# Kernel tuning notes

Hardware: AMD Instinct MI355X
Metric: run time of the kernel (lower is better)

## Reference

```python
import jax, jax.numpy as jnp
import numpy as np

B, H, S, DK = 2, 16, 2048, 64


def setup_inputs() -> dict:
    key = jax.random.key(0)
    k1, k2, k3, k4 = jax.random.split(key, 4)
    Q = jax.random.normal(k1, (B, H, S, DK), dtype=jnp.float32)
    K = jax.random.normal(k2, (B, H, S, DK), dtype=jnp.float32)
    V = jax.random.normal(k3, (B, H, S, DK), dtype=jnp.float32)
    attn_mask = jax.random.randint(k4, (B, 1, S, S), 0, 2).astype(jnp.bool_)
    return {"Q": Q, "K": K, "V": V, "attn_mask": attn_mask}


def reference(Q, K, V, attn_mask):
    d_k = Q.shape[-1]
    scale = 1.0 / jnp.sqrt(jnp.asarray(d_k, dtype=Q.dtype))
    # scores: [B,H,S,S]
    scores = jnp.einsum('bhqd,bhkd->bhqk', Q, K) * scale
    scores = jnp.where(attn_mask, jnp.asarray(-1e9, dtype=scores.dtype), scores)
    attn = jax.nn.softmax(scores, axis=-1)
    # dropout in eval mode (identity) for deterministic reference
    return jnp.einsum('bhqk,bhkd->bhqd', attn, V)
```

## Files before the change

### kernel.cpp

```cpp
#include <hip/hip_runtime.h>
#include <hip/hip_bf16.h>

#define Bdim 2
#define Hdim 16
#define Sdim 2048
#define Ddim 64
#define KVBLK 64
#define NT (Sdim / KVBLK)
#define WQ 32
#define NWAVE 4
#define QTILE (WQ * NWAVE)
#define QSCL (0.125f * 1.44269504088896f)
#define SCALE 0.125f
#define BUFE 8192
#define VOFF 4096

typedef __bf16 bf16x8 __attribute__((ext_vector_type(8)));
typedef float  f32x4  __attribute__((ext_vector_type(4)));
typedef float  f32x16 __attribute__((ext_vector_type(16)));
typedef unsigned u32x4 __attribute__((ext_vector_type(4)));

__device__ __forceinline__ void gll16(const __bf16* g, __bf16* l) {
  __builtin_amdgcn_global_load_lds(
      (const __attribute__((address_space(1))) void*)g,
      (__attribute__((address_space(3))) void*)l, 16, 0, 0);
}
__device__ __forceinline__ unsigned cvtpk_raw(float lo, float hi) {
  unsigned r;
  asm("v_cvt_pk_bf16_f32 %0, %1, %2" : "=v"(r) : "v"(lo), "v"(hi));
  return r;
}
template <bool SW>
__device__ __forceinline__ unsigned pko(float a, float b) {
  return SW ? cvtpk_raw(b, a) : cvtpk_raw(a, b);
}
__device__ __forceinline__ unsigned cvtpk(float a, float b, bool sw) {
  const float lo = sw ? b : a;
  const float hi = sw ? a : b;
  return cvtpk_raw(lo, hi);
}
template <bool SW>
__device__ __forceinline__ void packAll(const float (&sv0)[16],
                                        const float (&sv1)[16],
                                        unsigned (&pw)[16]) {
#pragma unroll
  for (int ks = 0; ks < 4; ++ks) {
    const int rb = 8 * (ks & 1);
    if (ks < 2) {
      pw[ks * 4 + 0] = pko<SW>(sv0[rb + 0], sv0[rb + 1]);
      pw[ks * 4 + 1] = pko<SW>(sv0[rb + 2], sv0[rb + 3]);
      pw[ks * 4 + 2] = pko<SW>(sv0[rb + 4], sv0[rb + 5]);
      pw[ks * 4 + 3] = pko<SW>(sv0[rb + 6], sv0[rb + 7]);
    } else {
      pw[ks * 4 + 0] = pko<SW>(sv1[rb + 0], sv1[rb + 1]);
      pw[ks * 4 + 1] = pko<SW>(sv1[rb + 2], sv1[rb + 3]);
      pw[ks * 4 + 2] = pko<SW>(sv1[rb + 4], sv1[rb + 5]);
      pw[ks * 4 + 3] = pko<SW>(sv1[rb + 6], sv1[rb + 7]);
    }
  }
}

__global__ __launch_bounds__(256) void prep_all(
    const void* __restrict__ mask, unsigned long long* __restrict__ packed,
    const float* __restrict__ K, const float* __restrict__ V,
    __bf16* __restrict__ Kb, __bf16* __restrict__ Vt) {
  __shared__ __bf16 tile[64][72];
  const int t = threadIdx.x;

  if (blockIdx.x < 512) {
    const int nwords = Bdim * Sdim * (Sdim / 64);
    const unsigned* m32 = (const unsigned*)mask;
    const unsigned char* m8 = (const unsigned char*)mask;
    int gid = blockIdx.x * 256 + t;
    int lane = gid & 63;
    int wid = gid >> 6;
    const int nwaves = 512 * 256 / 64;
    bool isBytes = __any(m32[lane] > 1u);
    for (int w = wid; w < nwords; w += nwaves) {
      int v = isBytes ? (int)m8[(size_t)w * 64 + lane]
                      : (int)m32[(size_t)w * 64 + lane];
      unsigned long long bal = __ballot(v != 0);
      if (lane == 0) packed[w] = bal;
    }
    return;
  }

  const int idx = blockIdx.x - 512;
  const int bh = idx >> 5, st = idx & 31;
  const int r = t >> 2, c0 = (t & 3) << 4;
  {
    const float* ks = K + ((size_t)bh * Sdim + st * 64 + r) * Ddim + c0;
    bf16x8 o0, o1;
#pragma unroll
    for (int j = 0; j < 8; ++j) o0[j] = (__bf16)ks[j];
#pragma unroll
    for (int j = 0; j < 8; ++j) o1[j] = (__bf16)ks[8 + j];
    __bf16* kd = Kb + ((size_t)bh * Sdim + st * 64 + r) * Ddim + c0;
    *(bf16x8*)kd = o0;
    *(bf16x8*)(kd + 8) = o1;
  }
  {
    const float* vs = V + ((size_t)bh * Sdim + st * 64 + r) * Ddim + c0;
#pragma unroll
    for (int j = 0; j < 16; ++j) tile[r][c0 + j] = (__bf16)vs[j];
  }
  __syncthreads();
  {
    const int d = t >> 2, s0 = (t & 3) << 4;
    __bf16 o[16];
#pragma unroll
    for (int j = 0; j < 16; ++j) o[j] = tile[s0 + j][d];
    __bf16* dst = Vt + ((size_t)bh * Ddim + d) * Sdim + st * 64 + s0;
    *(bf16x8*)dst = *(bf16x8*)&o[0];
    *(bf16x8*)(dst + 8) = *(bf16x8*)&o[8];
  }
}

__global__ __launch_bounds__(256, 2) void attn5(
    const float* __restrict__ Q, const __bf16* __restrict__ Kb,
    const __bf16* __restrict__ Vt,
    const unsigned long long* __restrict__ maskP, float* __restrict__ Out) {
  __shared__ alignas(16) __bf16 sm[4 * BUFE];

  const int tid = threadIdx.x;
  const int lane = tid & 63;
  const int w = tid >> 6;
  const int l31 = lane & 31;
  const int hi = lane >> 5;
  const int rsw = l31 & 7;

  const int bid = blockIdx.x;
  const int bh = bid & 31;
  const int qt = bid >> 5;
  const int b = bh >> 4;
  const int qrow = qt * QTILE + w * WQ + l31;

  const __bf16* Kbase = Kb + (size_t)bh * Sdim * Ddim;
  const __bf16* Vbase = Vt + (size_t)bh * (size_t)Ddim * Sdim;
  const unsigned long long* mp =
      maskP + ((size_t)b * Sdim + qrow) * (Sdim / 64);

  const bool sw = (cvtpk_raw(0.0f, 1.0f) & 0xFFFFu) != 0u;

  bf16x8 qf[4];
  {
    const float* qs = Q + ((size_t)bh * Sdim + qrow) * Ddim;
#pragma unroll
    for (int step = 0; step < 4; ++step) {
      const int d0 = step * 16 + hi * 8;
      float4 a = *(const float4*)(qs + d0);
      float4 c = *(const float4*)(qs + d0 + 4);
      u32x4 f;
      f[0] = cvtpk(a.x * QSCL, a.y * QSCL, sw);
      f[1] = cvtpk(a.z * QSCL, a.w * QSCL, sw);
      f[2] = cvtpk(c.x * QSCL, c.y * QSCL, sw);
      f[3] = cvtpk(c.z * QSCL, c.w * QSCL, sw);
      qf[step] = __builtin_bit_cast(bf16x8, f);
    }
  }

  const int srow = 16 * w + (lane >> 3);
  const int sblk = (lane & 7) ^ ((lane >> 3) & 7);
  const int dstw = w * 1024;

#define STAGE(OFFE, kp_, vp_)                                   \
  do {                                                          \
    gll16((kp_), &sm[(OFFE) + dstw]);                           \
    gll16((kp_) + 8 * Ddim, &sm[(OFFE) + dstw + 512]);          \
    gll16((vp_), &sm[(OFFE) + VOFF + dstw]);                    \
    gll16((vp_) + 8 * Sdim, &sm[(OFFE) + VOFF + dstw + 512]);   \
  } while (0)

  f32x16 otA = {0,0,0,0,0,0,0,0,0,0,0,0,0,0,0,0};
  f32x16 otB = {0,0,0,0,0,0,0,0,0,0,0,0,0,0,0,0};
  float lrow = 0.f;

  unsigned long long mwCur = mp[0];
  {
    const __bf16* kp0 = Kbase + (size_t)srow * Ddim + sblk * 8;
    const __bf16* vp0 = Vbase + (size_t)srow * Sdim + sblk * 8;
    STAGE(0, kp0, vp0);
  }
  const __bf16* kpS = Kbase + (size_t)(KVBLK + srow) * Ddim + sblk * 8;
  const __bf16* vpS = Vbase + (size_t)srow * Sdim + KVBLK + sblk * 8;

#define ITER(RD, ST, KTN, LAST)                                                \
  do {                                                                         \
    unsigned long long mwNext = 0;                                             \
    if (!(LAST)) {                                                             \
      mwNext = mp[(KTN)];                                                      \
      STAGE((ST) * BUFE, kpS, vpS);                                            \
      kpS += (size_t)KVBLK * Ddim;                                             \
      vpS += KVBLK;                                                            \
      asm volatile("s_waitcnt vmcnt(5)" ::: "memory");                         \
    } else {                                                                   \
      asm volatile("s_waitcnt vmcnt(0)" ::: "memory");                         \
    }                                                                          \
    __builtin_amdgcn_s_barrier();                                              \
    __builtin_amdgcn_sched_barrier(0);                                         \
    f32x16 st0 = {0,0,0,0,0,0,0,0,0,0,0,0,0,0,0,0};                            \
    f32x16 st1 = {0,0,0,0,0,0,0,0,0,0,0,0,0,0,0,0};                            \
    __builtin_amdgcn_s_setprio(1);                                             \
    _Pragma("unroll") for (int step = 0; step < 4; ++step) {                   \
      bf16x8 kf = *(const bf16x8*)&sm[(RD) * BUFE + l31 * 64 +                 \
                                      (((step * 2 + hi) ^ rsw) << 3)];         \
      st0 = __builtin_amdgcn_mfma_f32_32x32x16_bf16(kf, qf[step], st0, 0,0,0); \
    }                                                                          \
    _Pragma("unroll") for (int step = 0; step < 4; ++step) {                   \
      bf16x8 kf = *(const bf16x8*)&sm[(RD) * BUFE + (32 + l31) * 64 +          \
                                      (((step * 2 + hi) ^ rsw) << 3)];         \
      st1 = __builtin_amdgcn_mfma_f32_32x32x16_bf16(kf, qf[step], st1, 0,0,0); \
    }                                                                          \
    __builtin_amdgcn_s_setprio(0);                                             \
    float sv0[16], sv1[16];                                                    \
    const unsigned w0s = ((unsigned)mwCur) >> (hi * 4);                        \
    const unsigned w1s = ((unsigned)(mwCur >> 32)) >> (hi * 4);                \
    _Pragma("unroll") for (int r = 0; r < 16; ++r) {                           \
      const int cr = (r & 3) + 8 * (r >> 2);                                   \
      const float e0 = __builtin_amdgcn_exp2f(st0[r]);                         \
      const float e1 = __builtin_amdgcn_exp2f(st1[r]);                         \
      sv0[r] = ((w0s >> cr) & 1u) ? 0.f : e0;                                  \
      sv1[r] = ((w1s >> cr) & 1u) ? 0.f : e1;                                  \
    }                                                                          \
    float s8[8];                                                               \
    _Pragma("unroll") for (int j = 0; j < 8; ++j)                              \
      s8[j] = (sv0[j] + sv0[j + 8]) + (sv1[j] + sv1[j + 8]);                   \
    lrow += ((s8[0] + s8[4]) + (s8[1] + s8[5])) +                              \
            ((s8[2] + s8[6]) + (s8[3] + s8[7]));                               \
    unsigned pw[16];                                                           \
    if (!sw) packAll<false>(sv0, sv1, pw);                                     \
    else     packAll<true>(sv0, sv1, pw);                                      \
    bf16x8 pb[4];                                                              \
    _Pragma("unroll") for (int ks = 0; ks < 4; ++ks) {                         \
      const unsigned W0 = pw[ks * 4 + 0], W1 = pw[ks * 4 + 1];                 \
      const unsigned X0 = pw[ks * 4 + 2], X1 = pw[ks * 4 + 3];                 \
      const unsigned s1 = hi ? W0 : X0;                                        \
      const unsigned s2 = hi ? W1 : X1;                                        \
      const unsigned r1 = __shfl_xor(s1, 32, 64);                              \
      const unsigned r2 = __shfl_xor(s2, 32, 64);                              \
      u32x4 wv;                                                                \
      wv[0] = hi ? r1 : W0;                                                    \
      wv[1] = hi ? r2 : W1;                                                    \
      wv[2] = hi ? X0 : r1;                                                    \
      wv[3] = hi ? X1 : r2;                                                    \
      pb[ks] = __builtin_bit_cast(bf16x8, wv);                                 \
    }                                                                          \
    __builtin_amdgcn_s_setprio(1);                                             \
    _Pragma("unroll") for (int ks = 0; ks < 4; ++ks) {                         \
      bf16x8 vf = *(const bf16x8*)&sm[(RD) * BUFE + VOFF + l31 * 64 +          \
                                      (((ks * 2 + hi) ^ rsw) << 3)];           \
      otA = __builtin_amdgcn_mfma_f32_32x32x16_bf16(vf, pb[ks], otA, 0,0,0);   \
    }                                                                          \
    _Pragma("unroll") for (int ks = 0; ks < 4; ++ks) {                         \
      bf16x8 vf = *(const bf16x8*)&sm[(RD) * BUFE + VOFF + (32 + l31) * 64 +   \
                                      (((ks * 2 + hi) ^ rsw) << 3)];           \
      otB = __builtin_amdgcn_mfma_f32_32x32x16_bf16(vf, pb[ks], otB, 0,0,0);   \
    }                                                                          \
    __builtin_amdgcn_s_setprio(0);                                             \
    if (!(LAST)) mwCur = mwNext;                                               \
  } while (0)

#pragma unroll 1
  for (int g = 0; g < 7; ++g) {
    ITER(0, 1, 4 * g + 1, false);
    ITER(1, 2, 4 * g + 2, false);
    ITER(2, 3, 4 * g + 3, false);
    ITER(3, 0, 4 * g + 4, false);
  }
  ITER(0, 1, 29, false);
  ITER(1, 2, 30, false);
  ITER(2, 3, 31, false);
  ITER(3, 0, 0, true);
#undef ITER
#undef STAGE

  lrow += __shfl_xor(lrow, 32, 64);
  const float inv = 1.f / (lrow + 1e-30f);
  float* orow = Out + ((size_t)bh * Sdim + qrow) * Ddim;
#pragma unroll
  for (int g = 0; g < 4; ++g) {
    const int d0 = 8 * g + 4 * hi;
    float4 va = {otA[4 * g] * inv, otA[4 * g + 1] * inv,
                 otA[4 * g + 2] * inv, otA[4 * g + 3] * inv};
    float4 vb = {otB[4 * g] * inv, otB[4 * g + 1] * inv,
                 otB[4 * g + 2] * inv, otB[4 * g + 3] * inv};
    *(float4*)(orow + d0) = va;
    *(float4*)(orow + 32 + d0) = vb;
  }
}

__global__ __launch_bounds__(256) void attn_fallback(
    const float* __restrict__ Q, const float* __restrict__ K,
    const float* __restrict__ V, const void* __restrict__ maskRaw,
    float* __restrict__ Out) {
  __shared__ alignas(16) __bf16 Kl[KVBLK * Ddim];
  __shared__ alignas(16) __bf16 Vts[Ddim * KVBLK];
  __shared__ alignas(16) __bf16 Pl[4][16 * 64];

  const int tid = threadIdx.x;
  const int lane = tid & 63;
  const int w = tid >> 6;
  const int lhi = lane >> 4;
  const int llo = lane & 15;

  const int qt = blockIdx.x;
  const int bh = blockIdx.y;
  const int b = bh >> 4;
  const int qbase = qt * 64;

  const float* Qp = Q + (size_t)bh * Sdim * Ddim;
  const float* Kp = K + (size_t)bh * Sdim * Ddim;
  const float* Vp = V + (size_t)bh * Sdim * Ddim;

  bool maskBytes = __any(((const unsigned*)maskRaw)[lane] > 1u);

  bf16x8 qf0, qf1;
  {
    const int qr = qbase + w * 16 + llo;
    const float* src = Qp + (size_t)qr * Ddim + lhi * 8;
#pragma unroll
    for (int i = 0; i < 8; ++i) qf0[i] = (__bf16)(src[i] * SCALE);
#pragma unroll
    for (int i = 0; i < 8; ++i) qf1[i] = (__bf16)(src[32 + i] * SCALE);
  }

  f32x4 acc[4] = {{0.f,0.f,0.f,0.f},{0.f,0.f,0.f,0.f},
                  {0.f,0.f,0.f,0.f},{0.f,0.f,0.f,0.f}};
  float mrow[4], lrw[4];
#pragma unroll
  for (int r = 0; r < 4; ++r) { mrow[r] = -3.0e38f; lrw[r] = 0.f; }

  for (int kt = 0; kt < NT; ++kt) {
    __syncthreads();
    {
      int r = tid >> 2;
      int c0 = (tid & 3) << 4;
      const float* ks = Kp + (size_t)(kt * KVBLK + r) * Ddim + c0;
      const float* vs = Vp + (size_t)(kt * KVBLK + r) * Ddim + c0;
      float kv[16], vv[16];
#pragma unroll
      for (int j = 0; j < 4; ++j) {
        *(float4*)(&kv[j * 4]) = *(const float4*)(ks + j * 4);
        *(float4*)(&vv[j * 4]) = *(const float4*)(vs + j * 4);
      }
      const int swzK = (r & 7) << 3;
      bf16x8 k0v, k1v;
#pragma unroll
      for (int j = 0; j < 8; ++j) { k0v[j] = (__bf16)kv[j]; k1v[j] = (__bf16)kv[8 + j]; }
      *(bf16x8*)&Kl[r * 64 + (c0 ^ swzK)] = k0v;
      *(bf16x8*)&Kl[r * 64 + ((c0 + 8) ^ swzK)] = k1v;
#pragma unroll
      for (int j = 0; j < 16; ++j) {
        int d = c0 + j;
        Vts[d * 64 + (r ^ ((d & 7) << 3))] = (__bf16)vv[j];
      }
    }
    __syncthreads();

    float sv[4][4];
#pragma unroll
    for (int cb = 0; cb < 4; ++cb) {
      int krow = cb * 16 + llo;
      int swz = (krow & 7) << 3;
      bf16x8 kf0 = *(const bf16x8*)&Kl[krow * 64 + ((lhi * 8) ^ swz)];
      bf16x8 kf1 = *(const bf16x8*)&Kl[krow * 64 + ((32 + lhi * 8) ^ swz)];
      f32x4 s = {0.f, 0.f, 0.f, 0.f};
      s = __builtin_amdgcn_mfma_f32_16x16x32_bf16(qf0, kf0, s, 0, 0, 0);
      s = __builtin_amdgcn_mfma_f32_16x16x32_bf16(qf1, kf1, s, 0, 0, 0);
#pragma unroll
      for (int r = 0; r < 4; ++r) {
        size_t q = qbase + w * 16 + lhi * 4 + r;
        size_t k = (size_t)kt * KVBLK + cb * 16 + llo;
        size_t idx = ((size_t)b * Sdim + q) * Sdim + k;
        bool masked = maskBytes ? (((const unsigned char*)maskRaw)[idx] != 0)
                                : (((const int*)maskRaw)[idx] != 0);
        sv[cb][r] = masked ? -1e9f : s[r];
      }
    }

    float corr[4], tsum[4];
#pragma unroll
    for (int r = 0; r < 4; ++r) {
      float mx = fmaxf(fmaxf(sv[0][r], sv[1][r]), fmaxf(sv[2][r], sv[3][r]));
#pragma unroll
      for (int off = 1; off < 16; off <<= 1)
        mx = fmaxf(mx, __shfl_xor(mx, off, 64));
      float mnew = fmaxf(mrow[r], mx);
      corr[r] = __expf(mrow[r] - mnew);
      mrow[r] = mnew;
      tsum[r] = 0.f;
    }
#pragma unroll
    for (int cb = 0; cb < 4; ++cb) {
#pragma unroll
      for (int r = 0; r < 4; ++r) {
        float p = __expf(sv[cb][r] - mrow[r]);
        tsum[r] += p;
        int row = lhi * 4 + r;
        int col = cb * 16 + llo;
        Pl[w][row * 64 + (col ^ ((row & 7) << 3))] = (__bf16)p;
      }
    }
#pragma unroll
    for (int r = 0; r < 4; ++r) {
      float s = tsum[r];
#pragma unroll
      for (int off = 1; off < 16; off <<= 1)
        s += __shfl_xor(s, off, 64);
      lrw[r] = lrw[r] * corr[r] + s;
#pragma unroll
      for (int db = 0; db < 4; ++db) acc[db][r] *= corr[r];
    }
    asm volatile("s_waitcnt lgkmcnt(0)" ::: "memory");

    bf16x8 pf0 = *(const bf16x8*)&Pl[w][llo * 64 + ((lhi * 8) ^ ((llo & 7) << 3))];
    bf16x8 pf1 = *(const bf16x8*)&Pl[w][llo * 64 + ((32 + lhi * 8) ^ ((llo & 7) << 3))];
#pragma unroll
    for (int db = 0; db < 4; ++db) {
      int d = db * 16 + llo;
      int swz = (d & 7) << 3;
      bf16x8 vf0 = *(const bf16x8*)&Vts[d * 64 + ((lhi * 8) ^ swz)];
      bf16x8 vf1 = *(const bf16x8*)&Vts[d * 64 + ((32 + lhi * 8) ^ swz)];
      acc[db] = __builtin_amdgcn_mfma_f32_16x16x32_bf16(pf0, vf0, acc[db], 0, 0, 0);
      acc[db] = __builtin_amdgcn_mfma_f32_16x16x32_bf16(pf1, vf1, acc[db], 0, 0, 0);
    }
  }

#pragma unroll
  for (int r = 0; r < 4; ++r) {
    float inv = 1.f / lrw[r];
    int q = qbase + w * 16 + lhi * 4 + r;
    float* dst = Out + ((size_t)bh * Sdim + q) * Ddim + llo;
#pragma unroll
    for (int db = 0; db < 4; ++db) dst[db * 16] = acc[db][r] * inv;
  }
}

extern "C" void kernel_launch(void* const* d_in, const int* in_sizes, int n_in,
                              void* d_out, int out_size, void* d_ws, size_t ws_size,
                              hipStream_t stream) {
  const float* Q = (const float*)d_in[0];
  const float* K = (const float*)d_in[1];
  const float* V = (const float*)d_in[2];
  const void* mask = d_in[3];
  float* out = (float*)d_out;

  const size_t packed_bytes =
      (size_t)Bdim * Sdim * (Sdim / 64) * sizeof(unsigned long long);
  const size_t tensor_bf16 = (size_t)Bdim * Hdim * Sdim * Ddim * 2;

  if (ws_size >= packed_bytes + 2 * tensor_bf16) {
    unsigned long long* packed = (unsigned long long*)d_ws;
    __bf16* Kb = (__bf16*)((char*)d_ws + packed_bytes);
    __bf16* Vt = (__bf16*)((char*)d_ws + packed_bytes + tensor_bf16);
    prep_all<<<512 + Bdim * Hdim * (Sdim / 64), 256, 0, stream>>>(
        mask, packed, K, V, Kb, Vt);
    attn5<<<(Sdim / QTILE) * Bdim * Hdim, 256, 0, stream>>>(Q, Kb, Vt, packed, out);
  } else {
    attn_fallback<<<dim3(Sdim / 64, Bdim * Hdim), 256, 0, stream>>>(Q, K, V, mask, out);
  }
}
```

Before: 96.32 us.

## Give each wave private double-buffered K/V LDS staging and drop block barriers

```diff
diff --git a/kernel.cpp b/kernel.cpp
--- a/kernel.cpp
+++ b/kernel.cpp
@@ -5,15 +5,13 @@
 #define Hdim 16
 #define Sdim 2048
 #define Ddim 64
-#define KVBLK 64
-#define NT (Sdim / KVBLK)
+#define NT2 64
 #define WQ 32
 #define NWAVE 4
 #define QTILE (WQ * NWAVE)
 #define QSCL (0.125f * 1.44269504088896f)
 #define SCALE 0.125f
-#define BUFE 8192
-#define VOFF 4096
+#define WREG 8192
 
 typedef __bf16 bf16x8 __attribute__((ext_vector_type(8)));
 typedef float  f32x4  __attribute__((ext_vector_type(4)));
@@ -40,23 +38,15 @@
   return cvtpk_raw(lo, hi);
 }
 template <bool SW>
-__device__ __forceinline__ void packAll(const float (&sv0)[16],
-                                        const float (&sv1)[16],
-                                        unsigned (&pw)[16]) {
-#pragma unroll
-  for (int ks = 0; ks < 4; ++ks) {
-    const int rb = 8 * (ks & 1);
-    if (ks < 2) {
-      pw[ks * 4 + 0] = pko<SW>(sv0[rb + 0], sv0[rb + 1]);
-      pw[ks * 4 + 1] = pko<SW>(sv0[rb + 2], sv0[rb + 3]);
-      pw[ks * 4 + 2] = pko<SW>(sv0[rb + 4], sv0[rb + 5]);
-      pw[ks * 4 + 3] = pko<SW>(sv0[rb + 6], sv0[rb + 7]);
-    } else {
-      pw[ks * 4 + 0] = pko<SW>(sv1[rb + 0], sv1[rb + 1]);
-      pw[ks * 4 + 1] = pko<SW>(sv1[rb + 2], sv1[rb + 3]);
-      pw[ks * 4 + 2] = pko<SW>(sv1[rb + 4], sv1[rb + 5]);
-      pw[ks * 4 + 3] = pko<SW>(sv1[rb + 6], sv1[rb + 7]);
-    }
+__device__ __forceinline__ void packAll32(const float (&sv)[16],
+                                          unsigned (&pw)[8]) {
+#pragma unroll
+  for (int ks = 0; ks < 2; ++ks) {
+    const int rb = 8 * ks;
+    pw[ks * 4 + 0] = pko<SW>(sv[rb + 0], sv[rb + 1]);
+    pw[ks * 4 + 1] = pko<SW>(sv[rb + 2], sv[rb + 3]);
+    pw[ks * 4 + 2] = pko<SW>(sv[rb + 4], sv[rb + 5]);
+    pw[ks * 4 + 3] = pko<SW>(sv[rb + 6], sv[rb + 7]);
   }
 }
 
@@ -116,18 +106,17 @@
   }
 }
 
-__global__ __launch_bounds__(256, 2) void attn5(
+__global__ __launch_bounds__(256, 2) void attn7(
     const float* __restrict__ Q, const __bf16* __restrict__ Kb,
     const __bf16* __restrict__ Vt,
     const unsigned long long* __restrict__ maskP, float* __restrict__ Out) {
-  __shared__ alignas(16) __bf16 sm[4 * BUFE];
+  __shared__ alignas(16) __bf16 sm[NWAVE * WREG];
 
   const int tid = threadIdx.x;
   const int lane = tid & 63;
   const int w = tid >> 6;
   const int l31 = lane & 31;
   const int hi = lane >> 5;
-  const int rsw = l31 & 7;
 
   const int bid = blockIdx.x;
   const int bh = bid & 31;
@@ -137,8 +126,10 @@
 
   const __bf16* Kbase = Kb + (size_t)bh * Sdim * Ddim;
   const __bf16* Vbase = Vt + (size_t)bh * (size_t)Ddim * Sdim;
-  const unsigned long long* mp =
-      maskP + ((size_t)b * Sdim + qrow) * (Sdim / 64);
+  const unsigned* mp32 =
+      (const unsigned*)(maskP + ((size_t)b * Sdim + qrow) * (Sdim / 64));
+
+  __bf16* smw = sm + w * WREG;
 
   const bool sw = (cvtpk_raw(0.0f, 1.0f) & 0xFFFFu) != 0u;
 
@@ -159,79 +150,97 @@
     }
   }
 
-  const int srow = 16 * w + (lane >> 3);
-  const int sblk = (lane & 7) ^ ((lane >> 3) & 7);
-  const int dstw = w * 1024;
-
-#define STAGE(OFFE, kp_, vp_)                                   \
-  do {                                                          \
-    gll16((kp_), &sm[(OFFE) + dstw]);                           \
-    gll16((kp_) + 8 * Ddim, &sm[(OFFE) + dstw + 512]);          \
-    gll16((vp_), &sm[(OFFE) + VOFF + dstw]);                    \
-    gll16((vp_) + 8 * Sdim, &sm[(OFFE) + VOFF + dstw + 512]);   \
-  } while (0)
+  const int lr3 = lane >> 3;
+  const int ksb = (lane & 7) ^ lr3;
+  const int vbp = (lane & 7) ^ lr3;
+  const int vd0 = 2 * lr3 + (vbp >> 2);
+  const int vsc = vbp & 3;
+
+  const __bf16* kpS = Kbase + (size_t)lr3 * Ddim + ksb * 8;
+  const __bf16* vpS = Vbase + (size_t)vd0 * Sdim + vsc * 8;
+
+  const __bf16* kf[4];
+#pragma unroll
+  for (int s = 0; s < 4; ++s)
+    kf[s] = smw + l31 * 64 + (((s * 2 + hi) ^ (l31 & 7)) << 3);
+  const __bf16* vfp[2][2];
+#pragma unroll
+  for (int half = 0; half < 2; ++half)
+#pragma unroll
+    for (int ks = 0; ks < 2; ++ks)
+      vfp[half][ks] = smw + 2048 + half * 1024 + (l31 >> 1) * 64 +
+                      ((((l31 & 1) * 4 + ks * 2 + hi) ^ ((l31 >> 1) & 7)) << 3);
 
   f32x16 otA = {0,0,0,0,0,0,0,0,0,0,0,0,0,0,0,0};
   f32x16 otB = {0,0,0,0,0,0,0,0,0,0,0,0,0,0,0,0};
   float lrow = 0.f;
 
-  unsigned long long mwCur = mp[0];
-  {
-    const __bf16* kp0 = Kbase + (size_t)srow * Ddim + sblk * 8;
-    const __bf16* vp0 = Vbase + (size_t)srow * Sdim + sblk * 8;
-    STAGE(0, kp0, vp0);
-  }
-  const __bf16* kpS = Kbase + (size_t)(KVBLK + srow) * Ddim + sblk * 8;
-  const __bf16* vpS = Vbase + (size_t)srow * Sdim + KVBLK + sblk * 8;
-
-#define ITER(RD, ST, KTN, LAST)                                                \
+  unsigned mw32 = mp32[0];
+  const unsigned* mpp = mp32 + 1;
+  {
+    gll16(kpS, smw);
+    gll16(kpS + 8 * Ddim, smw + 512);
+    gll16(kpS + 16 * Ddim, smw + 1024);
+    gll16(kpS + 24 * Ddim, smw + 1536);
+    gll16(vpS, smw + 2048);
+    gll16(vpS + 16 * Sdim, smw + 2560);
+    gll16(vpS + 32 * Sdim, smw + 3072);
+    gll16(vpS + 48 * Sdim, smw + 3584);
+    kpS += 32 * Ddim;
+    vpS += 32;
+  }
+
+  unsigned mwNext;
+
+#define ITER2(BUFC, STBUF, LAST)                                               \
   do {                                                                         \
-    unsigned long long mwNext = 0;                                             \
     if (!(LAST)) {                                                             \
-      mwNext = mp[(KTN)];                                                      \
-      STAGE((ST) * BUFE, kpS, vpS);                                            \
-      kpS += (size_t)KVBLK * Ddim;                                             \
-      vpS += KVBLK;                                                            \
-      asm volatile("s_waitcnt vmcnt(5)" ::: "memory");                         \
+      mwNext = *mpp++;                                                         \
+      gll16(kpS, smw + (STBUF));                                               \
+      gll16(kpS + 8 * Ddim, smw + (STBUF) + 512);                              \
+      gll16(kpS + 16 * Ddim, smw + (STBUF) + 1024);                            \
+      gll16(kpS + 24 * Ddim, smw + (STBUF) + 1536);                            \
+      gll16(vpS, smw + (STBUF) + 2048);                                        \
+      gll16(vpS + 16 * Sdim, smw + (STBUF) + 2560);                            \
+      gll16(vpS + 32 * Sdim, smw + (STBUF) + 3072);                            \
+      gll16(vpS + 48 * Sdim, smw + (STBUF) + 3584);                            \
+      kpS += 32 * Ddim;                                                        \
+      vpS += 32;                                                               \
+       \
+      asm volatile("s_waitcnt vmcnt(9)" ::: "memory");                         \
     } else {                                                                   \
       asm volatile("s_waitcnt vmcnt(0)" ::: "memory");                         \
     }                                                                          \
-    __builtin_amdgcn_s_barrier();                                              \
     __builtin_amdgcn_sched_barrier(0);                                         \
-    f32x16 st0 = {0,0,0,0,0,0,0,0,0,0,0,0,0,0,0,0};                            \
-    f32x16 st1 = {0,0,0,0,0,0,0,0,0,0,0,0,0,0,0,0};                            \
+    f32x16 st = {0,0,0,0,0,0,0,0,0,0,0,0,0,0,0,0};                             \
     __builtin_amdgcn_s_setprio(1);                                             \
-    _Pragma("unroll") for (int step = 0; step < 4; ++step) {                   \
-      bf16x8 kf = *(const bf16x8*)&sm[(RD) * BUFE + l31 * 64 +                 \
-                                      (((step * 2 + hi) ^ rsw) << 3)];         \
-      st0 = __builtin_amdgcn_mfma_f32_32x32x16_bf16(kf, qf[step], st0, 0,0,0); \
-    }                                                                          \
-    _Pragma("unroll") for (int step = 0; step < 4; ++step) {                   \
-      bf16x8 kf = *(const bf16x8*)&sm[(RD) * BUFE + (32 + l31) * 64 +          \
-                                      (((step * 2 + hi) ^ rsw) << 3)];         \
-      st1 = __builtin_amdgcn_mfma_f32_32x32x16_bf16(kf, qf[step], st1, 0,0,0); \
-    }                                                                          \
+    st = __builtin_amdgcn_mfma_f32_32x32x16_bf16(                              \
+        *(const bf16x8*)(kf[0] + (BUFC)), qf[0], st, 0, 0, 0);                 \
+    st = __builtin_amdgcn_mfma_f32_32x32x16_bf16(                              \
+        *(const bf16x8*)(kf[1] + (BUFC)), qf[1], st, 0, 0, 0);                 \
+    st = __builtin_amdgcn_mfma_f32_32x32x16_bf16(                              \
+        *(const bf16x8*)(kf[2] + (BUFC)), qf[2], st, 0, 0, 0);                 \
+    st = __builtin_amdgcn_mfma_f32_32x32x16_bf16(                              \
+        *(const bf16x8*)(kf[3] + (BUFC)), qf[3], st, 0, 0, 0);                 \
     __builtin_amdgcn_s_setprio(0);                                             \
-    float sv0[16], sv1[16];                                                    \
-    const unsigned w0s = ((unsigned)mwCur) >> (hi * 4);                        \
-    const unsigned w1s = ((unsigned)(mwCur >> 32)) >> (hi * 4);                \
+    float sv[16];                                                              \
+    const unsigned ws_ = mw32 >> (hi * 4);                                     \
     _Pragma("unroll") for (int r = 0; r < 16; ++r) {                           \
       const int cr = (r & 3) + 8 * (r >> 2);                                   \
-      const float e0 = __builtin_amdgcn_exp2f(st0[r]);                         \
-      const float e1 = __builtin_amdgcn_exp2f(st1[r]);                         \
-      sv0[r] = ((w0s >> cr) & 1u) ? 0.f : e0;                                  \
-      sv1[r] = ((w1s >> cr) & 1u) ? 0.f : e1;                                  \
+      const float e0 = __builtin_amdgcn_exp2f(st[r]);                          \
+      sv[r] = ((ws_ >> cr) & 1u) ? 0.f : e0;                                   \
     }                                                                          \
-    float s8[8];                                                               \
-    _Pragma("unroll") for (int j = 0; j < 8; ++j)                              \
-      s8[j] = (sv0[j] + sv0[j + 8]) + (sv1[j] + sv1[j + 8]);                   \
-    lrow += ((s8[0] + s8[4]) + (s8[1] + s8[5])) +                              \
-            ((s8[2] + s8[6]) + (s8[3] + s8[7]));                               \
-    unsigned pw[16];                                                           \
-    if (!sw) packAll<false>(sv0, sv1, pw);                                     \
-    else     packAll<true>(sv0, sv1, pw);                                      \
-    bf16x8 pb[4];                                                              \
-    _Pragma("unroll") for (int ks = 0; ks < 4; ++ks) {                         \
+    {                                                                          \
+      float s8_[8];                                                            \
+      _Pragma("unroll") for (int j = 0; j < 8; ++j) s8_[j] = sv[j] + sv[j + 8];\
+      lrow += ((s8_[0] + s8_[4]) + (s8_[1] + s8_[5])) +                        \
+              ((s8_[2] + s8_[6]) + (s8_[3] + s8_[7]));                         \
+    }                                                                          \
+    unsigned pw[8];                                                            \
+    if (!sw) packAll32<false>(sv, pw);                                         \
+    else     packAll32<true>(sv, pw);                                          \
+    bf16x8 pb[2];                                                              \
+    _Pragma("unroll") for (int ks = 0; ks < 2; ++ks) {                         \
       const unsigned W0 = pw[ks * 4 + 0], W1 = pw[ks * 4 + 1];                 \
       const unsigned X0 = pw[ks * 4 + 2], X1 = pw[ks * 4 + 3];                 \
       const unsigned s1 = hi ? W0 : X0;                                        \
@@ -246,33 +255,26 @@
       pb[ks] = __builtin_bit_cast(bf16x8, wv);                                 \
     }                                                                          \
     __builtin_amdgcn_s_setprio(1);                                             \
-    _Pragma("unroll") for (int ks = 0; ks < 4; ++ks) {                         \
-      bf16x8 vf = *(const bf16x8*)&sm[(RD) * BUFE + VOFF + l31 * 64 +          \
-                                      (((ks * 2 + hi) ^ rsw) << 3)];           \
-      otA = __builtin_amdgcn_mfma_f32_32x32x16_bf16(vf, pb[ks], otA, 0,0,0);   \
-    }                                                                          \
-    _Pragma("unroll") for (int ks = 0; ks < 4; ++ks) {                         \
-      bf16x8 vf = *(const bf16x8*)&sm[(RD) * BUFE + VOFF + (32 + l31) * 64 +   \
-                                      (((ks * 2 + hi) ^ rsw) << 3)];           \
-      otB = __builtin_amdgcn_mfma_f32_32x32x16_bf16(vf, pb[ks], otB, 0,0,0);   \
-    }                                                                          \
+    otA = __builtin_amdgcn_mfma_f32_32x32x16_bf16(                             \
+        *(const bf16x8*)(vfp[0][0] + (BUFC)), pb[0], otA, 0, 0, 0);            \
+    otA = __builtin_amdgcn_mfma_f32_32x32x16_bf16(                             \
+        *(const bf16x8*)(vfp[0][1] + (BUFC)), pb[1], otA, 0, 0, 0);            \
+    otB = __builtin_amdgcn_mfma_f32_32x32x16_bf16(                             \
+        *(const bf16x8*)(vfp[1][0] + (BUFC)), pb[0], otB, 0, 0, 0);            \
+    otB = __builtin_amdgcn_mfma_f32_32x32x16_bf16(                             \
+        *(const bf16x8*)(vfp[1][1] + (BUFC)), pb[1], otB, 0, 0, 0);            \
     __builtin_amdgcn_s_setprio(0);                                             \
-    if (!(LAST)) mwCur = mwNext;                                               \
+    mw32 = mwNext;                                                             \
   } while (0)
 
 #pragma unroll 1
-  for (int g = 0; g < 7; ++g) {
-    ITER(0, 1, 4 * g + 1, false);
-    ITER(1, 2, 4 * g + 2, false);
-    ITER(2, 3, 4 * g + 3, false);
-    ITER(3, 0, 4 * g + 4, false);
-  }
-  ITER(0, 1, 29, false);
-  ITER(1, 2, 30, false);
-  ITER(2, 3, 31, false);
-  ITER(3, 0, 0, true);
-#undef ITER
-#undef STAGE
+  for (int g = 0; g < 31; ++g) {
+    ITER2(0, 4096, false);
+    ITER2(4096, 0, false);
+  }
+  ITER2(0, 4096, false);
+  ITER2(4096, 0, true);
+#undef ITER2
 
   lrow += __shfl_xor(lrow, 32, 64);
   const float inv = 1.f / (lrow + 1e-30f);
@@ -293,8 +295,8 @@
     const float* __restrict__ Q, const float* __restrict__ K,
     const float* __restrict__ V, const void* __restrict__ maskRaw,
     float* __restrict__ Out) {
-  __shared__ alignas(16) __bf16 Kl[KVBLK * Ddim];
-  __shared__ alignas(16) __bf16 Vts[Ddim * KVBLK];
+  __shared__ alignas(16) __bf16 Kl[64 * Ddim];
+  __shared__ alignas(16) __bf16 Vts[Ddim * 64];
   __shared__ alignas(16) __bf16 Pl[4][16 * 64];
 
   const int tid = threadIdx.x;
@@ -330,13 +332,13 @@
 #pragma unroll
   for (int r = 0; r < 4; ++r) { mrow[r] = -3.0e38f; lrw[r] = 0.f; }
 
-  for (int kt = 0; kt < NT; ++kt) {
+  for (int kt = 0; kt < Sdim / 64; ++kt) {
     __syncthreads();
     {
       int r = tid >> 2;
       int c0 = (tid & 3) << 4;
-      const float* ks = Kp + (size_t)(kt * KVBLK + r) * Ddim + c0;
-      const float* vs = Vp + (size_t)(kt * KVBLK + r) * Ddim + c0;
+      const float* ks = Kp + (size_t)(kt * 64 + r) * Ddim + c0;
+      const float* vs = Vp + (size_t)(kt * 64 + r) * Ddim + c0;
       float kv[16], vv[16];
 #pragma unroll
       for (int j = 0; j < 4; ++j) {
@@ -370,7 +372,7 @@
 #pragma unroll
       for (int r = 0; r < 4; ++r) {
         size_t q = qbase + w * 16 + lhi * 4 + r;
-        size_t k = (size_t)kt * KVBLK + cb * 16 + llo;
+        size_t k = (size_t)kt * 64 + cb * 16 + llo;
         size_t idx = ((size_t)b * Sdim + q) * Sdim + k;
         bool masked = maskBytes ? (((const unsigned char*)maskRaw)[idx] != 0)
                                 : (((const int*)maskRaw)[idx] != 0);
@@ -455,7 +457,7 @@
     __bf16* Vt = (__bf16*)((char*)d_ws + packed_bytes + tensor_bf16);
     prep_all<<<512 + Bdim * Hdim * (Sdim / 64), 256, 0, stream>>>(
         mask, packed, K, V, Kb, Vt);
-    attn5<<<(Sdim / QTILE) * Bdim * Hdim, 256, 0, stream>>>(Q, Kb, Vt, packed, out);
+    attn7<<<(Sdim / QTILE) * Bdim * Hdim, 256, 0, stream>>>(Q, Kb, Vt, packed, out);
   } else {
     attn_fallback<<<dim3(Sdim / 64, Bdim * Hdim), 256, 0, stream>>>(Q, K, V, mask, out);
   }
```

Result: slower. 111.3 us (+15.6%).
